# Kernel optimization log

Measured on AMD Instinct MI355X. Metric: run time of the kernel, lower is better.

Reference implementation:

```python
import jax, jax.numpy as jnp
import numpy as np

B, N, I, O, H = 4, 2047, 256, 128, 4
NEG = -1e18
SLOPE = 0.2


def setup_inputs() -> dict:
    key = jax.random.key(0)
    ks = jax.random.split(key, 8)
    x = jax.random.normal(ks[0], (B, N, I), dtype=jnp.float32)
    prior_feature = jax.random.normal(ks[1], (B, O), dtype=jnp.float32)
    x_mask = jax.random.randint(ks[2], (B, N + 1), 0, 2).astype(bool)
    # learned parameters (xavier-ish scaling)
    W_lin = jax.random.normal(ks[3], (O, I), dtype=jnp.float32) * (1.0 / np.sqrt(I))
    w_head = jax.random.normal(ks[4], (H, O, O), dtype=jnp.float32) * (1.0 / np.sqrt(O))
    a_src = jax.random.normal(ks[5], (H, O), dtype=jnp.float32) * (1.0 / np.sqrt(O))
    a_dst = jax.random.normal(ks[6], (H, O), dtype=jnp.float32) * (1.0 / np.sqrt(O))
    bias = jnp.zeros((O,), dtype=jnp.float32)
    return {"x": x, "prior_feature": prior_feature, "x_mask": x_mask,
            "W_lin": W_lin, "w_head": w_head, "a_src": a_src, "a_dst": a_dst, "bias": bias}


def reference(x, prior_feature, x_mask, W_lin, w_head, a_src, a_dst, bias):
    # self_linear (no bias), then concat prior feature as extra node -> [B, N1, O]
    h = jnp.einsum('bni,oi->bno', x, W_lin)
    hp = jnp.concatenate([h, prior_feature[:, None, :]], axis=1)  # [B, N1, O]
    # per-head projection: [B,1,N1,O] @ [H,O,O] -> [B,H,N1,O]
    hp = jnp.einsum('bno,hop->bhnp', hp, w_head)
    t = jnp.tanh(hp)
    s_src = jnp.einsum('bhno,ho->bhn', t, a_src)  # [B,H,N1]
    s_dst = jnp.einsum('bhno,ho->bhn', t, a_dst)  # [B,H,N1]
    attn = s_src[..., :, None] + s_dst[..., None, :]  # [B,H,N1,N1]
    attn = jnp.where(attn >= 0, attn, SLOPE * attn)  # leaky_relu(0.2)
    mask = x_mask[:, :, None] | x_mask[:, None, :]    # [B,N1,N1]
    attn = jnp.where(mask[:, None, :, :], jnp.float32(NEG), attn)
    attn = jax.nn.softmax(attn, axis=-1)
    # dropout p=0.0 -> identity
    out = jnp.einsum('bhij,bhjo->bhio', attn, hp) + bias  # [B,H,N1,O]
    return out.mean(axis=1)  # mean over heads -> [B,N1,O]
```

## Files before the change

kernel.cpp:

```cpp
#include <hip/hip_runtime.h>
#include <hip/hip_bf16.h>
#include <cmath>


#define B_ 4
#define N_ 2047
#define N1 2048
#define I_ 256
#define O_ 128
#define H_ 4
#define NBINS 256
#define STR 132
#define SLOPEC 0.2f
#define HS_STR 136
#define XS_STR 72

typedef unsigned short u16;
typedef unsigned char u8;
typedef short bf16x8 __attribute__((ext_vector_type(8)));
typedef float f32x4 __attribute__((ext_vector_type(4)));
#define MFMA16(a,b,c) __builtin_amdgcn_mfma_f32_16x16x32_bf16(a,b,c,0,0,0)

__device__ __forceinline__ float bf2f(u16 v){
  union { unsigned u; float f; } x; x.u = ((unsigned)v) << 16; return x.f;
}
__device__ __forceinline__ u16 f2bf(float f){
  union { float f; unsigned u; } x; x.f = f;
  unsigned u = x.u;
  return (u16)((u + 0x7FFFu + ((u >> 16) & 1u)) >> 16);
}
__device__ __forceinline__ float ldv(const void* p, int bf, size_t i){
  if (bf) return bf2f(reinterpret_cast<const u16*>(p)[i]);
  return reinterpret_cast<const float*>(p)[i];
}
__device__ __forceinline__ void ld8(const void* p, int bf, size_t i, float* o){
  if (bf){
    uint4 v = *reinterpret_cast<const uint4*>(reinterpret_cast<const u16*>(p) + i);
    o[0]=bf2f((u16)(v.x&0xFFFF)); o[1]=bf2f((u16)(v.x>>16));
    o[2]=bf2f((u16)(v.y&0xFFFF)); o[3]=bf2f((u16)(v.y>>16));
    o[4]=bf2f((u16)(v.z&0xFFFF)); o[5]=bf2f((u16)(v.z>>16));
    o[6]=bf2f((u16)(v.w&0xFFFF)); o[7]=bf2f((u16)(v.w>>16));
  } else {
    const float4* q = reinterpret_cast<const float4*>(reinterpret_cast<const float*>(p) + i);
    float4 a = q[0], b = q[1];
    o[0]=a.x; o[1]=a.y; o[2]=a.z; o[3]=a.w;
    o[4]=b.x; o[5]=b.y; o[6]=b.z; o[7]=b.w;
  }
}
__device__ __forceinline__ void st8bf(u16* dst, const void* src, int bf, size_t i){
  if (bf){
    *reinterpret_cast<uint4*>(dst) =
      *reinterpret_cast<const uint4*>(reinterpret_cast<const u16*>(src) + i);
  } else {
    float v[8]; ld8(src, 0, i, v);
    u16 tmp[8];
#pragma unroll
    for (int m = 0; m < 8; m++) tmp[m] = f2bf(v[m]);
    *reinterpret_cast<uint4*>(dst) = *reinterpret_cast<uint4*>(tmp);
  }
}
__device__ __forceinline__ float clS(float v){ return fminf(30.f, fmaxf(-30.f, v)); }
__device__ __forceinline__ float clH(float v){ return fminf(1e4f, fmaxf(-1e4f, v)); }
__device__ __forceinline__ int binOf(float v, float lo, float inv){
  int c = (int)((v - lo) * inv);
  c = c < 0 ? 0 : c;
  c = c > NBINS - 1 ? NBINS - 1 : c;
  return c;
}
__device__ __forceinline__ int rdmask(const u8* m, int mode, int idx){
  return mode ? (m[idx] != 0) : (((const int*)m)[idx] != 0);
}

__global__ __launch_bounds__(1024) void k0_detect(const u8* __restrict__ mask,
                                                  const void* x, const void* prior,
                                                  const void* Wlin, const void* wh,
                                                  const void* asr, const void* ads,
                                                  int* __restrict__ flags,
                                                  float* __restrict__ colsum){
  __shared__ int c[8];
  const int t = threadIdx.x;
  for (int i = t; i < B_ * H_ * O_; i += 1024) colsum[i] = 0.f;
  if (t < 8) c[t] = 0;
  __syncthreads();
  int local = 0;
  for (int i = t; i < B_ * N1; i += 1024)
    if ((i & 3) && mask[i]) local = 1;
  if (local) atomicOr(&c[0], 1);
  const void* ptrs[6] = {x, prior, Wlin, wh, asr, ads};
  const int   lens[6] = {4096, 512, 4096, 4096, 512, 512};
  for (int k = 0; k < 6; k++){
    const u16* p = (const u16*)ptrs[k];
    int g = 0;
    for (int i = t; i < lens[k]; i += 1024){
      int e = (p[i] >> 7) & 0xFF;
      if (e >= 0xC0) g++;
    }
    if (g) atomicAdd(&c[k + 1], g);
  }
  __syncthreads();
  if (t == 0) flags[0] = c[0];
  else if (t <= 6) flags[t] = (c[t] < 4) ? 1 : 0;
}

__global__ __launch_bounds__(256) void ktr(const void* __restrict__ w_head,
                                           const int* __restrict__ flags,
                                           u16* __restrict__ wT){
  const int fw = flags[4];
  const int idx = blockIdx.x * 256 + threadIdx.x;
  const int h = idx >> 14, rem = idx & 16383, p = rem >> 7, o = rem & 127;
  wT[idx] = f2bf(ldv(w_head, fw, ((size_t)h * O_ + o) * O_ + p));
}

__global__ __launch_bounds__(256) void k1_hp(const void* __restrict__ x,
                                             const void* __restrict__ prior,
                                             const void* __restrict__ Wlin,
                                             const int* __restrict__ flags,
                                             u16* __restrict__ hpb){
  __shared__ __align__(16) u16 xs[32 * XS_STR];
  __shared__ __align__(16) u16 wl[128 * XS_STR];
  const int fx = flags[1], fpf = flags[2], fw = flags[3];
  const int tile = blockIdx.x & 63;
  const int b    = blockIdx.x >> 6;
  const int n0   = tile * 32;
  const int t = threadIdx.x;
  const int w = t >> 6, lane = t & 63, m16 = lane & 15, q = lane >> 4;
  const int rbase = (w & 1) * 16;
  const int cbase = (w >> 1) * 64;
  f32x4 acc[4];
#pragma unroll
  for (int nt = 0; nt < 4; nt++) acc[nt] = (f32x4){0.f, 0.f, 0.f, 0.f};
  for (int kt = 0; kt < I_; kt += 64){
    if (kt) __syncthreads();
    {
      const int row = t >> 3, ch = t & 7;
      const int n = n0 + row;
      if (n < N_) st8bf(&xs[row * XS_STR + ch * 8], x, fx, ((size_t)b * N_ + n) * I_ + kt + ch * 8);
      else { uint4 z = make_uint4(0,0,0,0); *reinterpret_cast<uint4*>(&xs[row * XS_STR + ch * 8]) = z; }
    }
#pragma unroll
    for (int it = 0; it < 4; it++){
      const int slot = t + it * 256, row = slot >> 3, ch = slot & 7;
      st8bf(&wl[row * XS_STR + ch * 8], Wlin, fw, (size_t)row * I_ + kt + ch * 8);
    }
    __syncthreads();
#pragma unroll
    for (int ks = 0; ks < 2; ks++){
      const int k0 = ks * 32 + q * 8;
      const bf16x8 af = *reinterpret_cast<const bf16x8*>(&xs[(rbase + m16) * XS_STR + k0]);
#pragma unroll
      for (int nt = 0; nt < 4; nt++){
        const bf16x8 bfr = *reinterpret_cast<const bf16x8*>(&wl[(cbase + nt * 16 + m16) * XS_STR + k0]);
        acc[nt] = MFMA16(af, bfr, acc[nt]);
      }
    }
  }
#pragma unroll
  for (int nt = 0; nt < 4; nt++){
#pragma unroll
    for (int r = 0; r < 4; r++){
      const int n = n0 + rbase + q * 4 + r;
      const int col = cbase + nt * 16 + m16;
      const float v = (n == N_) ? ldv(prior, fpf, b * O_ + col) : acc[nt][r];
      hpb[((size_t)b * N1 + n) * O_ + col] = f2bf(v);
    }
  }
}

__global__ __launch_bounds__(256) void k2_heads(const u16* __restrict__ hpb,
                                                const u16* __restrict__ wT,
                                                const void* __restrict__ a_src,
                                                const void* __restrict__ a_dst,
                                                const int* __restrict__ flags,
                                                float* __restrict__ hph,
                                                float* __restrict__ s_src,
                                                float* __restrict__ s_dst,
                                                float* __restrict__ colsum){
  __shared__ __align__(16) u16 hsb[64 * HS_STR];
  __shared__ __align__(16) u16 wtb[128 * HS_STR];
  __shared__ float colacc[O_];
  const int fas = flags[5], fad = flags[6];
  const int tile = blockIdx.x & 31;
  const int h    = (blockIdx.x >> 5) & 3;
  const int b    = blockIdx.x >> 7;
  const int bh   = b * H_ + h;
  const int n0   = tile * 64;
  const int t = threadIdx.x;
  const int w = t >> 6, lane = t & 63, m16 = lane & 15, q = lane >> 4;
  if (t < O_) colacc[t] = 0.f;
#pragma unroll
  for (int it = 0; it < 4; it++){
    const int slot = t + it * 256, row = slot >> 4, ch = slot & 15;
    *reinterpret_cast<uint4*>(&hsb[row * HS_STR + ch * 8]) =
      *reinterpret_cast<const uint4*>(&hpb[((size_t)b * N1 + n0 + row) * O_ + ch * 8]);
  }
#pragma unroll
  for (int it = 0; it < 8; it++){
    const int slot = t + it * 256, row = slot >> 4, ch = slot & 15;
    *reinterpret_cast<uint4*>(&wtb[row * HS_STR + ch * 8]) =
      *reinterpret_cast<const uint4*>(&wT[((size_t)h * O_ + row) * O_ + ch * 8]);
  }
  __syncthreads();
  f32x4 acc[8];
#pragma unroll
  for (int nt = 0; nt < 8; nt++) acc[nt] = (f32x4){0.f, 0.f, 0.f, 0.f};
#pragma unroll
  for (int ks = 0; ks < 4; ks++){
    const int k0 = ks * 32 + q * 8;
    const bf16x8 af = *reinterpret_cast<const bf16x8*>(&hsb[(w * 16 + m16) * HS_STR + k0]);
#pragma unroll
    for (int nt = 0; nt < 8; nt++){
      const bf16x8 bfr = *reinterpret_cast<const bf16x8*>(&wtb[(nt * 16 + m16) * HS_STR + k0]);
      acc[nt] = MFMA16(af, bfr, acc[nt]);
    }
  }
  float ps[4] = {0.f, 0.f, 0.f, 0.f}, pd[4] = {0.f, 0.f, 0.f, 0.f};
#pragma unroll
  for (int nt = 0; nt < 8; nt++){
    const int col = nt * 16 + m16;
    const float asv = ldv(a_src, fas, h * O_ + col);
    const float adv = ldv(a_dst, fad, h * O_ + col);
    float colpart = 0.f;
#pragma unroll
    for (int r = 0; r < 4; r++){
      const float v = clH(acc[nt][r]);
      hph[((size_t)bh * N1 + n0 + w * 16 + q * 4 + r) * O_ + col] = v;
      colpart += v;
      const float tv = tanhf(v);
      ps[r] += tv * asv;
      pd[r] += tv * adv;
    }
    atomicAdd(&colacc[col], colpart);
  }
#pragma unroll
  for (int r = 0; r < 4; r++){
#pragma unroll
    for (int m = 8; m > 0; m >>= 1){
      ps[r] += __shfl_xor(ps[r], m);
      pd[r] += __shfl_xor(pd[r], m);
    }
    if (m16 == 0){
      const int n = n0 + w * 16 + q * 4 + r;
      s_src[(size_t)bh * N1 + n] = ps[r];
      s_dst[(size_t)bh * N1 + n] = pd[r];
    }
  }
  __syncthreads();
  if (t < O_) atomicAdd(&colsum[bh * O_ + t], colacc[t]);
}

__global__ __launch_bounds__(256) void k3a_bucket(const float* __restrict__ s_dst,
                                                  const u8* __restrict__ mask,
                                                  const int* __restrict__ flags,
                                                  float* __restrict__ sdlo,
                                                  float* __restrict__ sdinv,
                                                  int* __restrict__ binStart,
                                                  int* __restrict__ order){
  __shared__ float smn[4], smx[4];
  __shared__ float sli[2];
  __shared__ int cnt[NBINS];
  __shared__ int part[256];
  __shared__ int offs[256 + 1];
  const int bh = blockIdx.x, b = bh / H_, t = threadIdx.x;
  const int md = flags[0];
  float mn = 3e38f, mx = -3e38f;
  for (int j = t; j < N1; j += 256){
    if (!rdmask(mask, md, b * N1 + j)){
      float v = clS(s_dst[(size_t)bh * N1 + j]);
      mn = fminf(mn, v); mx = fmaxf(mx, v);
    }
  }
#pragma unroll
  for (int sft = 32; sft > 0; sft >>= 1){
    mn = fminf(mn, __shfl_down(mn, sft));
    mx = fmaxf(mx, __shfl_down(mx, sft));
  }
  if ((t & 63) == 0){ smn[t >> 6] = mn; smx[t >> 6] = mx; }
  __syncthreads();
  if (t == 0){
    mn = fminf(fminf(smn[0], smn[1]), fminf(smn[2], smn[3]));
    mx = fmaxf(fmaxf(smx[0], smx[1]), fmaxf(smx[2], smx[3]));
    float range = mx - mn;
    if (!(range > 1e-30f)) range = 1.f;
    const float inv = (float)NBINS / range;
    sdlo[bh]  = mn;
    sdinv[bh] = inv;
    sli[0] = mn; sli[1] = inv;
  }
  __syncthreads();
  const float lo = sli[0], inv = sli[1];
  cnt[t] = 0;
  __syncthreads();
  for (int j = t; j < N1; j += 256){
    if (!rdmask(mask, md, b * N1 + j))
      atomicAdd(&cnt[binOf(clS(s_dst[(size_t)bh * N1 + j]), lo, inv)], 1);
  }
  __syncthreads();
  const int mysum = cnt[t];
  part[t] = mysum;
  __syncthreads();
  for (int off = 1; off < 256; off <<= 1){
    int v = (t >= off) ? part[t - off] : 0;
    __syncthreads();
    part[t] += v;
    __syncthreads();
  }
  const int excl = part[t] - mysum;
  offs[t] = excl;
  binStart[bh * (NBINS + 1) + t] = excl;
  if (t == 255) binStart[bh * (NBINS + 1) + NBINS] = part[255];
  __syncthreads();
  for (int j = t; j < N1; j += 256){
    if (!rdmask(mask, md, b * N1 + j)){
      int bin = binOf(clS(s_dst[(size_t)bh * N1 + j]), lo, inv);
      int pos = atomicAdd(&offs[bin], 1);
      order[(size_t)bh * N1 + pos] = j;
    }
  }
}

__global__ __launch_bounds__(192) void k3b_binsum(const float* __restrict__ hph,
                                                  const float* __restrict__ s_dst,
                                                  const int* __restrict__ binStart,
                                                  const int* __restrict__ order,
                                                  float* __restrict__ binPos,
                                                  float* __restrict__ binNeg){
  __shared__ int jls[64];
  __shared__ float fpl[64], fnl[64];
  const int gb = blockIdx.x;
  const int bh = gb / NBINS, bin = gb % NBINS;
  const int t = threadIdx.x;
  const int s = binStart[bh * (NBINS + 1) + bin];
  const int e = binStart[bh * (NBINS + 1) + bin + 1];
  float ap = 0.f, an = 0.f;
  for (int mb = s; mb < e; mb += 64){
    const int cn = min(64, e - mb);
    if (t < cn){
      const int j = order[(size_t)bh * N1 + mb + t];
      const float sdj = clS(s_dst[(size_t)bh * N1 + j]);
      jls[t] = j;
      fpl[t] = __expf(sdj);
      fnl[t] = __expf(SLOPEC * sdj);
    }
    __syncthreads();
    for (int m = 0; m < cn; m++){
      const float v = (t < O_) ? hph[((size_t)bh * N1 + jls[m]) * O_ + t] : 1.f;
      ap += fpl[m] * v;
      an += fnl[m] * v;
    }
    __syncthreads();
  }
  if (t <= O_){
    const size_t basei = ((size_t)bh * NBINS + bin) * STR;
    binPos[basei + t] = ap;
    binNeg[basei + t] = an;
  }
}

__global__ __launch_bounds__(256) void k3c1(const float* __restrict__ binPos,
                                            const float* __restrict__ binNeg,
                                            float* __restrict__ chunkSum){
  const int idx = blockIdx.x * 256 + threadIdx.x;
  if (idx >= 2 * 16 * 4 * 129) return;
  const int ch = idx % 129;
  int rest = idx / 129;
  const int chunk = rest & 3;
  rest >>= 2;
  const int bh = rest & 15;
  const int arr = rest >> 4;
  const float* src = arr ? binPos : binNeg;
  float s = 0.f;
  const size_t base = ((size_t)bh * NBINS + chunk * 64) * STR + ch;
  for (int r = 0; r < 64; r++) s += src[base + (size_t)r * STR];
  chunkSum[(((size_t)arr * 16 + bh) * 4 + chunk) * STR + ch] = s;
}

__global__ __launch_bounds__(256) void k3c2(const float* __restrict__ binPos,
                                            const float* __restrict__ binNeg,
                                            const float* __restrict__ chunkSum,
                                            float* __restrict__ sufPos,
                                            float* __restrict__ preNeg){
  const int idx = blockIdx.x * 256 + threadIdx.x;
  if (idx >= 2 * 16 * 4 * 129) return;
  const int ch = idx % 129;
  int rest = idx / 129;
  const int chunk = rest & 3;
  rest >>= 2;
  const int bh = rest & 15;
  const int arr = rest >> 4;
  if (arr == 0){
    float acc = 0.f;
    for (int cc = 0; cc < chunk; cc++)
      acc += chunkSum[(((size_t)bh) * 4 + cc) * STR + ch];
    for (int rr = 0; rr < 64; rr++){
      const int r = chunk * 64 + rr;
      preNeg[((size_t)bh * (NBINS + 1) + r) * STR + ch] = acc;
      acc += binNeg[((size_t)bh * NBINS + r) * STR + ch];
    }
    if (chunk == 3) preNeg[((size_t)bh * (NBINS + 1) + NBINS) * STR + ch] = acc;
  } else {
    float acc = 0.f;
    for (int cc = chunk + 1; cc < 4; cc++)
      acc += chunkSum[(((size_t)16 + bh) * 4 + cc) * STR + ch];
    for (int rr = 63; rr >= 0; rr--){
      const int r = chunk * 64 + rr;
      acc += binPos[((size_t)bh * NBINS + r) * STR + ch];
      sufPos[((size_t)bh * (NBINS + 1) + r) * STR + ch] = acc;
    }
    if (chunk == 3) sufPos[((size_t)bh * (NBINS + 1) + NBINS) * STR + ch] = 0.f;
  }
}

__global__ __launch_bounds__(512) void k3d_out(const float* __restrict__ hph,
                                               const float* __restrict__ s_src,
                                               const float* __restrict__ s_dst,
                                               const u8* __restrict__ mask,
                                               const int* __restrict__ flags,
                                               const float* __restrict__ sdlo,
                                               const float* __restrict__ sdinv,
                                               const int* __restrict__ binStart,
                                               const int* __restrict__ order,
                                               const float* __restrict__ sufPos,
                                               const float* __restrict__ preNeg,
                                               const float* __restrict__ colsum,
                                               const void* __restrict__ bias,
                                               void* __restrict__ outp){
  __shared__ float part[4 * STR];
  const int blk = blockIdx.x;
  const int b = blk >> 11, i = blk & (N1 - 1);
  const int t = threadIdx.x;
  const int h = t >> 7, o = t & 127;
  const int lane = t & 63;
  const int md = flags[0], fo = flags[1];
  const int bh = b * H_ + h;
  const int U = binStart[bh * (NBINS + 1) + NBINS];
  const bool mrow = rdmask(mask, md, b * N1 + i) != 0;
  float contrib;
  if (mrow || U == 0){
    contrib = colsum[bh * O_ + o] * (1.f / N1);
  } else {
    const float si = clS(s_src[(size_t)bh * N1 + i]);
    const float tthr = -si;
    const int c = binOf(tthr, sdlo[bh], sdinv[bh]);
    const size_t rowp = ((size_t)bh * (NBINS + 1) + c + 1) * STR;
    const size_t rown = ((size_t)bh * (NBINS + 1) + c) * STR;
    float posV = sufPos[rowp + o], posS = sufPos[rowp + O_];
    float negV = preNeg[rown + o], negS = preNeg[rown + O_];
    const int s0 = binStart[bh * (NBINS + 1) + c];
    const int e0 = binStart[bh * (NBINS + 1) + c + 1];
    for (int mb = s0; mb < e0; mb += 64){
      const int cn = min(64, e0 - mb);
      int jm = 0; float sdm = 0.f, fpm = 0.f, fnm = 0.f;
      if (lane < cn){
        jm = order[(size_t)bh * N1 + mb + lane];
        sdm = clS(s_dst[(size_t)bh * N1 + jm]);
        fpm = __expf(sdm);
        fnm = __expf(SLOPEC * sdm);
      }
      int m = 0;
      for (; m + 3 < cn; m += 4){
        const int j0 = __shfl(jm, m),     j1 = __shfl(jm, m + 1);
        const int j2 = __shfl(jm, m + 2), j3 = __shfl(jm, m + 3);
        const float hv0 = hph[((size_t)bh * N1 + j0) * O_ + o];
        const float hv1 = hph[((size_t)bh * N1 + j1) * O_ + o];
        const float hv2 = hph[((size_t)bh * N1 + j2) * O_ + o];
        const float hv3 = hph[((size_t)bh * N1 + j3) * O_ + o];
        const float sd0 = __shfl(sdm, m),     sd1 = __shfl(sdm, m + 1);
        const float sd2 = __shfl(sdm, m + 2), sd3 = __shfl(sdm, m + 3);
        const float fp0 = __shfl(fpm, m),     fp1 = __shfl(fpm, m + 1);
        const float fp2 = __shfl(fpm, m + 2), fp3 = __shfl(fpm, m + 3);
        const float fn0 = __shfl(fnm, m),     fn1 = __shfl(fnm, m + 1);
        const float fn2 = __shfl(fnm, m + 2), fn3 = __shfl(fnm, m + 3);
        if (sd0 >= tthr){ posV += fp0 * hv0; posS += fp0; } else { negV += fn0 * hv0; negS += fn0; }
        if (sd1 >= tthr){ posV += fp1 * hv1; posS += fp1; } else { negV += fn1 * hv1; negS += fn1; }
        if (sd2 >= tthr){ posV += fp2 * hv2; posS += fp2; } else { negV += fn2 * hv2; negS += fn2; }
        if (sd3 >= tthr){ posV += fp3 * hv3; posS += fp3; } else { negV += fn3 * hv3; negS += fn3; }
      }
      for (; m < cn; m++){
        const int j = __shfl(jm, m);
        const float sdj = __shfl(sdm, m);
        const float fp = __shfl(fpm, m);
        const float fn = __shfl(fnm, m);
        const float hv = hph[((size_t)bh * N1 + j) * O_ + o];
        if (sdj >= tthr){ posV += fp * hv; posS += fp; }
        else            { negV += fn * hv; negS += fn; }
      }
    }
    const float esi = __expf(si), esi2 = __expf(SLOPEC * si);
    const float den = fmaxf(esi * posS + esi2 * negS, 1e-35f);
    contrib = (esi * posV + esi2 * negV) / den;
  }
  part[h * STR + o] = contrib;
  __syncthreads();
  if (t < O_){
    const float sum = part[0 * STR + t] + part[1 * STR + t] + part[2 * STR + t] + part[3 * STR + t];
    const float v = 0.25f * sum + ldv(bias, fo, t);
    const size_t oidx = ((size_t)b * N1 + i) * O_ + t;
    if (fo) ((u16*)outp)[oidx] = f2bf(v);
    else    ((float*)outp)[oidx] = v;
  }
}

extern "C" void kernel_launch(void* const* d_in, const int* in_sizes, int n_in,
                              void* d_out, int out_size, void* d_ws, size_t ws_size,
                              hipStream_t stream){
  const void* x      = d_in[0];
  const void* prior  = d_in[1];
  const u8*   mask   = (const u8*)d_in[2];
  const void* Wlin   = d_in[3];
  const void* w_head = d_in[4];
  const void* a_src  = d_in[5];
  const void* a_dst  = d_in[6];
  const void* bias   = d_in[7];

  char* basep = (char*)d_ws;
  size_t off = 0;
  auto alloc = [&](size_t bytes) -> void* {
    off = (off + 255) & ~(size_t)255;
    void* p = basep + off;
    off += bytes;
    return p;
  };
  int*   flags    = (int*)alloc(32);
  u16*   wT       = (u16*)alloc((size_t)H_ * O_ * O_ * 2);
  u16*   hpb      = (u16*)alloc((size_t)B_ * N1 * O_ * 2);
  float* hph      = (float*)alloc((size_t)B_ * H_ * N1 * O_ * 4);
  float* s_src    = (float*)alloc((size_t)B_ * H_ * N1 * 4);
  float* s_dst    = (float*)alloc((size_t)B_ * H_ * N1 * 4);
  float* sdlo     = (float*)alloc(B_ * H_ * 4);
  float* sdinv    = (float*)alloc(B_ * H_ * 4);
  float* colsum   = (float*)alloc((size_t)B_ * H_ * O_ * 4);
  int*   binStart = (int*)alloc((size_t)B_ * H_ * (NBINS + 1) * 4);
  int*   order    = (int*)alloc((size_t)B_ * H_ * N1 * 4);
  float* binPos   = (float*)alloc((size_t)B_ * H_ * NBINS * STR * 4);
  float* binNeg   = (float*)alloc((size_t)B_ * H_ * NBINS * STR * 4);
  float* sufPos   = (float*)alloc((size_t)B_ * H_ * (NBINS + 1) * STR * 4);
  float* preNeg   = (float*)alloc((size_t)B_ * H_ * (NBINS + 1) * STR * 4);
  float* chunkSum = (float*)alloc((size_t)2 * 16 * 4 * STR * 4);
  (void)in_sizes; (void)n_in; (void)out_size; (void)ws_size;

  const int scanN = 2 * 16 * 4 * 129;
  hipLaunchKernelGGL(k0_detect,  dim3(1),                   dim3(1024), 0, stream, mask, x, prior, Wlin, w_head, a_src, a_dst, flags, colsum);
  hipLaunchKernelGGL(ktr,        dim3(256),                 dim3(256), 0, stream, w_head, flags, wT);
  hipLaunchKernelGGL(k1_hp,      dim3(B_ * 64),             dim3(256), 0, stream, x, prior, Wlin, flags, hpb);
  hipLaunchKernelGGL(k2_heads,   dim3(B_ * H_ * 32),        dim3(256), 0, stream, hpb, wT, a_src, a_dst, flags, hph, s_src, s_dst, colsum);
  hipLaunchKernelGGL(k3a_bucket, dim3(B_ * H_),             dim3(256), 0, stream, s_dst, mask, flags, sdlo, sdinv, binStart, order);
  hipLaunchKernelGGL(k3b_binsum, dim3(B_ * H_ * NBINS),     dim3(192), 0, stream, hph, s_dst, binStart, order, binPos, binNeg);
  hipLaunchKernelGGL(k3c1,       dim3((scanN + 255) / 256), dim3(256), 0, stream, binPos, binNeg, chunkSum);
  hipLaunchKernelGGL(k3c2,       dim3((scanN + 255) / 256), dim3(256), 0, stream, binPos, binNeg, chunkSum, sufPos, preNeg);
  hipLaunchKernelGGL(k3d_out,    dim3(B_ * N1),             dim3(512), 0, stream, hph, s_src, s_dst, mask, flags, sdlo, sdinv, binStart, order, sufPos, preNeg, colsum, bias, d_out);
}
```

Before: 161.2 us.

## Double bucket count to 512 and fuse two-pass bin scan into one kernel

Raises the number of s_dst histogram bins from 256 to 512, so each bin holds fewer nodes and the per-query correction work in the output kernel shrinks. The bucket kernel now handles two bins per thread in its prefix scan. The two scan kernels (chunk sums, then prefix/suffix) are merged into one kernel that keeps the chunk sums in shared memory, removing a launch and a global round trip. In exchange the bin-sum and prefix/suffix arrays double in size, and k3b launches twice as many blocks, each with less work.

```diff
diff --git a/kernel.cpp b/kernel.cpp
--- a/kernel.cpp
+++ b/kernel.cpp
@@ -9,7 +9,9 @@
 #define I_ 256
 #define O_ 128
 #define H_ 4
-#define NBINS 256
+#define NBINS 512
+#define NCHUNK 4
+#define CBINS (NBINS / NCHUNK)
 #define STR 132
 #define SLOPEC 0.2f
 #define HS_STR 136
@@ -259,7 +261,7 @@
   __shared__ float sli[2];
   __shared__ int cnt[NBINS];
   __shared__ int part[256];
-  __shared__ int offs[256 + 1];
+  __shared__ int offs[NBINS];
   const int bh = blockIdx.x, b = bh / H_, t = threadIdx.x;
   const int md = flags[0];
   float mn = 3e38f, mx = -3e38f;
@@ -288,14 +290,15 @@
   }
   __syncthreads();
   const float lo = sli[0], inv = sli[1];
-  cnt[t] = 0;
+  cnt[t] = 0; cnt[t + 256] = 0;
   __syncthreads();
   for (int j = t; j < N1; j += 256){
     if (!rdmask(mask, md, b * N1 + j))
       atomicAdd(&cnt[binOf(clS(s_dst[(size_t)bh * N1 + j]), lo, inv)], 1);
   }
   __syncthreads();
-  const int mysum = cnt[t];
+  const int s0 = cnt[2 * t], s1 = cnt[2 * t + 1];
+  const int mysum = s0 + s1;
   part[t] = mysum;
   __syncthreads();
   for (int off = 1; off < 256; off <<= 1){
@@ -305,8 +308,10 @@
     __syncthreads();
   }
   const int excl = part[t] - mysum;
-  offs[t] = excl;
-  binStart[bh * (NBINS + 1) + t] = excl;
+  offs[2 * t] = excl;
+  offs[2 * t + 1] = excl + s0;
+  binStart[bh * (NBINS + 1) + 2 * t] = excl;
+  binStart[bh * (NBINS + 1) + 2 * t + 1] = excl + s0;
   if (t == 255) binStart[bh * (NBINS + 1) + NBINS] = part[255];
   __syncthreads();
   for (int j = t; j < N1; j += 256){
@@ -356,57 +361,45 @@
   }
 }
 
-__global__ __launch_bounds__(256) void k3c1(const float* __restrict__ binPos,
-                                            const float* __restrict__ binNeg,
-                                            float* __restrict__ chunkSum){
-  const int idx = blockIdx.x * 256 + threadIdx.x;
-  if (idx >= 2 * 16 * 4 * 129) return;
-  const int ch = idx % 129;
-  int rest = idx / 129;
-  const int chunk = rest & 3;
-  rest >>= 2;
-  const int bh = rest & 15;
-  const int arr = rest >> 4;
+__global__ __launch_bounds__(576) void k3c_scan(const float* __restrict__ binPos,
+                                                const float* __restrict__ binNeg,
+                                                float* __restrict__ sufPos,
+                                                float* __restrict__ preNeg){
+  __shared__ float csum[NCHUNK][132];
+  const int blk = blockIdx.x;
+  const int bh = blk & 15, arr = blk >> 4;
+  const int t = threadIdx.x;
+  const bool act = t < NCHUNK * 129;
+  const int ch = act ? (t % 129) : 0;
+  const int chunk = act ? (t / 129) : 0;
   const float* src = arr ? binPos : binNeg;
-  float s = 0.f;
-  const size_t base = ((size_t)bh * NBINS + chunk * 64) * STR + ch;
-  for (int r = 0; r < 64; r++) s += src[base + (size_t)r * STR];
-  chunkSum[(((size_t)arr * 16 + bh) * 4 + chunk) * STR + ch] = s;
-}
-
-__global__ __launch_bounds__(256) void k3c2(const float* __restrict__ binPos,
-                                            const float* __restrict__ binNeg,
-                                            const float* __restrict__ chunkSum,
-                                            float* __restrict__ sufPos,
-                                            float* __restrict__ preNeg){
-  const int idx = blockIdx.x * 256 + threadIdx.x;
-  if (idx >= 2 * 16 * 4 * 129) return;
-  const int ch = idx % 129;
-  int rest = idx / 129;
-  const int chunk = rest & 3;
-  rest >>= 2;
-  const int bh = rest & 15;
-  const int arr = rest >> 4;
-  if (arr == 0){
-    float acc = 0.f;
-    for (int cc = 0; cc < chunk; cc++)
-      acc += chunkSum[(((size_t)bh) * 4 + cc) * STR + ch];
-    for (int rr = 0; rr < 64; rr++){
-      const int r = chunk * 64 + rr;
-      preNeg[((size_t)bh * (NBINS + 1) + r) * STR + ch] = acc;
-      acc += binNeg[((size_t)bh * NBINS + r) * STR + ch];
-    }
-    if (chunk == 3) preNeg[((size_t)bh * (NBINS + 1) + NBINS) * STR + ch] = acc;
-  } else {
-    float acc = 0.f;
-    for (int cc = chunk + 1; cc < 4; cc++)
-      acc += chunkSum[(((size_t)16 + bh) * 4 + cc) * STR + ch];
-    for (int rr = 63; rr >= 0; rr--){
-      const int r = chunk * 64 + rr;
-      acc += binPos[((size_t)bh * NBINS + r) * STR + ch];
-      sufPos[((size_t)bh * (NBINS + 1) + r) * STR + ch] = acc;
-    }
-    if (chunk == 3) sufPos[((size_t)bh * (NBINS + 1) + NBINS) * STR + ch] = 0.f;
+  if (act){
+    float s = 0.f;
+    const size_t base = ((size_t)bh * NBINS + chunk * CBINS) * STR + ch;
+    for (int r = 0; r < CBINS; r++) s += src[base + (size_t)r * STR];
+    csum[chunk][ch] = s;
+  }
+  __syncthreads();
+  if (act){
+    if (arr == 0){
+      float acc = 0.f;
+      for (int cc = 0; cc < chunk; cc++) acc += csum[cc][ch];
+      for (int rr = 0; rr < CBINS; rr++){
+        const int r = chunk * CBINS + rr;
+        preNeg[((size_t)bh * (NBINS + 1) + r) * STR + ch] = acc;
+        acc += binNeg[((size_t)bh * NBINS + r) * STR + ch];
+      }
+      if (chunk == NCHUNK - 1) preNeg[((size_t)bh * (NBINS + 1) + NBINS) * STR + ch] = acc;
+    } else {
+      float acc = 0.f;
+      for (int cc = chunk + 1; cc < NCHUNK; cc++) acc += csum[cc][ch];
+      for (int rr = CBINS - 1; rr >= 0; rr--){
+        const int r = chunk * CBINS + rr;
+        acc += binPos[((size_t)bh * NBINS + r) * STR + ch];
+        sufPos[((size_t)bh * (NBINS + 1) + r) * STR + ch] = acc;
+      }
+      if (chunk == NCHUNK - 1) sufPos[((size_t)bh * (NBINS + 1) + NBINS) * STR + ch] = 0.f;
+    }
   }
 }
 
@@ -535,17 +528,14 @@
   float* binNeg   = (float*)alloc((size_t)B_ * H_ * NBINS * STR * 4);
   float* sufPos   = (float*)alloc((size_t)B_ * H_ * (NBINS + 1) * STR * 4);
   float* preNeg   = (float*)alloc((size_t)B_ * H_ * (NBINS + 1) * STR * 4);
-  float* chunkSum = (float*)alloc((size_t)2 * 16 * 4 * STR * 4);
   (void)in_sizes; (void)n_in; (void)out_size; (void)ws_size;
 
-  const int scanN = 2 * 16 * 4 * 129;
-  hipLaunchKernelGGL(k0_detect,  dim3(1),                   dim3(1024), 0, stream, mask, x, prior, Wlin, w_head, a_src, a_dst, flags, colsum);
-  hipLaunchKernelGGL(ktr,        dim3(256),                 dim3(256), 0, stream, w_head, flags, wT);
-  hipLaunchKernelGGL(k1_hp,      dim3(B_ * 64),             dim3(256), 0, stream, x, prior, Wlin, flags, hpb);
-  hipLaunchKernelGGL(k2_heads,   dim3(B_ * H_ * 32),        dim3(256), 0, stream, hpb, wT, a_src, a_dst, flags, hph, s_src, s_dst, colsum);
-  hipLaunchKernelGGL(k3a_bucket, dim3(B_ * H_),             dim3(256), 0, stream, s_dst, mask, flags, sdlo, sdinv, binStart, order);
-  hipLaunchKernelGGL(k3b_binsum, dim3(B_ * H_ * NBINS),     dim3(192), 0, stream, hph, s_dst, binStart, order, binPos, binNeg);
-  hipLaunchKernelGGL(k3c1,       dim3((scanN + 255) / 256), dim3(256), 0, stream, binPos, binNeg, chunkSum);
-  hipLaunchKernelGGL(k3c2,       dim3((scanN + 255) / 256), dim3(256), 0, stream, binPos, binNeg, chunkSum, sufPos, preNeg);
-  hipLaunchKernelGGL(k3d_out,    dim3(B_ * N1),             dim3(512), 0, stream, hph, s_src, s_dst, mask, flags, sdlo, sdinv, binStart, order, sufPos, preNeg, colsum, bias, d_out);
-}
+  hipLaunchKernelGGL(k0_detect,  dim3(1),                dim3(1024), 0, stream, mask, x, prior, Wlin, w_head, a_src, a_dst, flags, colsum);
+  hipLaunchKernelGGL(ktr,        dim3(256),              dim3(256), 0, stream, w_head, flags, wT);
+  hipLaunchKernelGGL(k1_hp,      dim3(B_ * 64),          dim3(256), 0, stream, x, prior, Wlin, flags, hpb);
+  hipLaunchKernelGGL(k2_heads,   dim3(B_ * H_ * 32),     dim3(256), 0, stream, hpb, wT, a_src, a_dst, flags, hph, s_src, s_dst, colsum);
+  hipLaunchKernelGGL(k3a_bucket, dim3(B_ * H_),          dim3(256), 0, stream, s_dst, mask, flags, sdlo, sdinv, binStart, order);
+  hipLaunchKernelGGL(k3b_binsum, dim3(B_ * H_ * NBINS),  dim3(192), 0, stream, hph, s_dst, binStart, order, binPos, binNeg);
+  hipLaunchKernelGGL(k3c_scan,   dim3(32),               dim3(576), 0, stream, binPos, binNeg, sufPos, preNeg);
+  hipLaunchKernelGGL(k3d_out,    dim3(B_ * N1),          dim3(512), 0, stream, hph, s_src, s_dst, mask, flags, sdlo, sdinv, binStart, order, sufPos, preNeg, colsum, bias, d_out);
+}
```

New measurement: 162.9 us. About the same (+1.1%).
